# Kernel tuning notes

Hardware: AMD Instinct MI355X
Metric: run time of the kernel (lower is better)

Reference implementation:

```python
import jax, jax.numpy as jnp
import numpy as np

D_MODEL = 512
NUM_HEADS = 8
D_HEAD = D_MODEL // NUM_HEADS
SCALE = 1.0 / np.sqrt(D_HEAD)


def setup_inputs() -> dict:
    key = jax.random.key(0)
    ks = jax.random.split(key, 16)
    B, T, D = 8, 1024, D_MODEL
    std = 1.0 / np.sqrt(D)
    inp = {
        'x': jax.random.normal(ks[0], (B, T, D), jnp.float32),
        'pos_enc': jax.random.normal(ks[1], (1, 2 * T - 1, D), jnp.float32),
        'Wq': jax.random.normal(ks[2], (D, D), jnp.float32) * std,
        'bq': jnp.zeros((D,), jnp.float32),
        'Wk': jax.random.normal(ks[3], (D, D), jnp.float32) * std,
        'bk': jnp.zeros((D,), jnp.float32),
        'Wv': jax.random.normal(ks[4], (D, D), jnp.float32) * std,
        'bv': jnp.zeros((D,), jnp.float32),
        'Wpos': jax.random.normal(ks[5], (D, D), jnp.float32) * std,
        'pos_bias_u': jax.random.normal(ks[6], (NUM_HEADS, D_HEAD), jnp.float32) * std,
        'pos_bias_v': jax.random.normal(ks[7], (NUM_HEADS, D_HEAD), jnp.float32) * std,
        'Wo': jax.random.normal(ks[8], (D, D), jnp.float32) * std,
        'bo': jnp.zeros((D,), jnp.float32),
    }
    return inp


def _relative_shift(x):
    # x: (batch, heads, time, 2*time-1) -> (batch, heads, time, time)
    b, h, t, _ = x.shape
    x = jnp.pad(x, ((0, 0), (0, 0), (0, 0), (1, 0)))  # (b,h,t,2t)
    x = x.reshape(b, h, 2 * t, t)
    x = x[:, :, 1:, :]
    x = x.reshape(b, h, t, 2 * t - 1)
    return x[:, :, :, :t]


def reference(x, pos_enc, Wq, bq, Wk, bk, Wv, bv, Wpos, pos_bias_u, pos_bias_v, Wo, bo):
    B, T, D = x.shape
    H, Dh = NUM_HEADS, D_HEAD
    q = (x @ Wq + bq).reshape(B, T, H, Dh).transpose(0, 2, 1, 3)  # (B,H,T,Dh)
    k = (x @ Wk + bk).reshape(B, T, H, Dh).transpose(0, 2, 1, 3)
    v = (x @ Wv + bv).reshape(B, T, H, Dh).transpose(0, 2, 1, 3)
    p = (pos_enc @ Wpos).reshape(1, -1, H, Dh).transpose(0, 2, 1, 3)  # (1,H,2T-1,Dh)

    q_u = q + pos_bias_u[None, :, None, :]
    q_v = q + pos_bias_v[None, :, None, :]

    content_score = jnp.einsum('bhtd,bhsd->bhts', q_u, k)         # (B,H,T,T)
    pos_score = jnp.einsum('bhtd,xhpd->bhtp', q_v, p)             # (B,H,T,2T-1)
    pos_score = _relative_shift(pos_score)                         # (B,H,T,T)

    scores = (content_score + pos_score) * SCALE
    attn = jax.nn.softmax(scores, axis=-1)
    out = jnp.einsum('bhts,bhsd->bhtd', attn, v)                   # (B,H,T,Dh)
    out = out.transpose(0, 2, 1, 3).reshape(B, T, D)
    return out @ Wo + bo
```

## Files before the change

kernel.cpp:

```cpp
#include <hip/hip_runtime.h>
#include <hip/hip_bf16.h>

#define T_SEQ 1024
#define D_MODEL 512
#define N_HEADS 8
#define D_HEAD 64
#define KSCALE 0.1803368801111244f

typedef unsigned short ushort_t;
typedef short s16x8 __attribute__((ext_vector_type(8)));
typedef float f32x4 __attribute__((ext_vector_type(4)));

__device__ inline f32x4 mfma16(s16x8 a, s16x8 b, f32x4 c) {
    return __builtin_amdgcn_mfma_f32_16x16x32_bf16(a, b, c, 0, 0, 0);
}

__device__ inline ushort_t f2bf(float f) {
    union { float f; unsigned u; } v; v.f = f;
    unsigned r = v.u + 0x7FFFu + ((v.u >> 16) & 1u);
    return (ushort_t)(r >> 16);
}
__device__ inline float bf2f(short s) {
    union { unsigned u; float f; } t; t.u = ((unsigned)(unsigned short)s) << 16; return t.f;
}
__device__ inline void cvt4(const float4 f, ushort_t* t) {
    t[0] = f2bf(f.x); t[1] = f2bf(f.y); t[2] = f2bf(f.z); t[3] = f2bf(f.w);
}
__device__ inline s16x8 pack8(const ushort_t* t) {
    s16x8 r;
    #pragma unroll
    for (int e = 0; e < 8; ++e) r[e] = (short)t[e];
    return r;
}

__device__ inline int lidx(int row, int chunk) {
    return row * 64 + ((chunk ^ (row & 7)) << 3);
}

__device__ inline void gl_lds16(const ushort_t* g, ushort_t* l) {
    __builtin_amdgcn_global_load_lds(
        (const __attribute__((address_space(1))) unsigned*)g,
        (__attribute__((address_space(3))) unsigned*)l, 16, 0, 0);
}

__global__ __launch_bounds__(256) void prep(
    const float* __restrict__ x, const float* __restrict__ pos,
    const float* __restrict__ W0, const float* __restrict__ W1,
    const float* __restrict__ W2, const float* __restrict__ W3,
    const float* __restrict__ W4,
    ushort_t* __restrict__ xb, ushort_t* __restrict__ posb,
    ushort_t* __restrict__ WT)
{
    __shared__ float T[64][68];
    const int bx = blockIdx.x;
    const int tid = threadIdx.x;
    if (bx < 2560) {
        const size_t N1 = (size_t)8192 * 512;
        size_t e = ((size_t)bx * 256 + tid) * 8;
        ushort_t tmp[8];
        if (e < N1) {
            const float4* s = (const float4*)(x + e);
            cvt4(s[0], tmp); cvt4(s[1], tmp + 4);
            *(s16x8*)(xb + e) = pack8(tmp);
        } else {
            size_t e2 = e - N1;
            int row = (int)(e2 >> 9);
            if (row < 2047) {
                const float4* s = (const float4*)(pos + e2);
                cvt4(s[0], tmp); cvt4(s[1], tmp + 4);
            } else {
                #pragma unroll
                for (int i = 0; i < 8; ++i) tmp[i] = 0;
            }
            *(s16x8*)(posb + e2) = pack8(tmp);
        }
    } else {
        const int bz = bx - 2560;
        const int z = bz >> 6;
        const int rem = bz & 63;
        const int n0 = (rem & 7) * 64, k0 = (rem >> 3) * 64;
        const float* W = (z == 0) ? W0 : (z == 1) ? W1
                       : (z == 2) ? W2 : (z == 3) ? W3 : W4;
        const int rr = tid >> 2, cc = (tid & 3) * 16;

        const float* src = W + (size_t)(k0 + rr) * 512 + n0 + cc;
        *(float4*)&T[rr][cc + 0]  = *(const float4*)(src);
        *(float4*)&T[rr][cc + 4]  = *(const float4*)(src + 4);
        *(float4*)&T[rr][cc + 8]  = *(const float4*)(src + 8);
        *(float4*)&T[rr][cc + 12] = *(const float4*)(src + 12);
        __syncthreads();

        ushort_t tmp[16];
        #pragma unroll
        for (int e = 0; e < 16; ++e) tmp[e] = f2bf(T[cc + e][rr]);
        ushort_t* dst = WT + ((size_t)z * 512 + n0 + rr) * 512 + k0 + cc;
        *(s16x8*)dst       = pack8(tmp);
        *(s16x8*)(dst + 8) = pack8(tmp + 8);
    }
}

__global__ __launch_bounds__(256) void gemm_qkvp(
    const ushort_t* __restrict__ xb, const ushort_t* __restrict__ posb,
    const ushort_t* __restrict__ WT,
    const float* __restrict__ bq, const float* __restrict__ bk,
    const float* __restrict__ bv, const float* __restrict__ pbu,
    ushort_t* __restrict__ Qu, ushort_t* __restrict__ Ko,
    ushort_t* __restrict__ VoT, ushort_t* __restrict__ Po)
{
    const int tid = threadIdx.x;
    const int flat = blockIdx.x;
    const int nf = (flat & 7) * 104 + (flat >> 3);
    const int bxi = nf % 13, byi = nf / 13;

    const bool is_p = (bxi == 12);
    int row0, col0;
    const ushort_t* A;
    const ushort_t* B;
    if (is_p) {
        row0 = (byi >> 2) * 128;
        col0 = (byi & 3) * 128;
        A = posb;
        B = WT + (size_t)3 * 512 * 512;
    } else {
        row0 = byi * 128;
        col0 = bxi * 128;
        A = xb;
        B = WT;
    }
    const int w = tid >> 6, lane = tid & 63;
    const int quad = lane >> 4, lanelo = lane & 15;
    const int wr = w >> 1, wc = w & 1;

    __shared__ ushort_t AsF[128 * 64];
    __shared__ ushort_t BsF[128 * 64];

    f32x4 acc[4][4] = {};

    for (int k0 = 0; k0 < 512; k0 += 64) {
        __syncthreads();
        #pragma unroll
        for (int i = 0; i < 4; ++i) {
            const int L = i * 256 + tid;
            const int r = L >> 3, j = (L & 7) * 8;
            ushort_t* lbase = AsF + (size_t)(i * 256 + (tid & ~63)) * 8;
            gl_lds16(A + (size_t)(row0 + r) * 512 + k0 + j, lbase);
            ushort_t* lbase2 = BsF + (size_t)(i * 256 + (tid & ~63)) * 8;
            gl_lds16(B + (size_t)(col0 + r) * 512 + k0 + j, lbase2);
        }
        __syncthreads();

        #pragma unroll
        for (int ks = 0; ks < 2; ++ks) {
            s16x8 af[4], bf[4];
            #pragma unroll
            for (int i = 0; i < 4; ++i)
                af[i] = *(const s16x8*)(AsF + (size_t)(64 * wr + 16 * i + lanelo) * 64 + ks * 32 + quad * 8);
            #pragma unroll
            for (int j = 0; j < 4; ++j)
                bf[j] = *(const s16x8*)(BsF + (size_t)(64 * wc + 16 * j + lanelo) * 64 + ks * 32 + quad * 8);
            #pragma unroll
            for (int i = 0; i < 4; ++i)
                #pragma unroll
                for (int j = 0; j < 4; ++j)
                    acc[i][j] = mfma16(af[i], bf[j], acc[i][j]);
        }
    }

    if (is_p) {
        #pragma unroll
        for (int j = 0; j < 4; ++j) {
            int c = col0 + 64 * wc + 16 * j + lanelo;
            #pragma unroll
            for (int i = 0; i < 4; ++i)
                #pragma unroll
                for (int r = 0; r < 4; ++r) {
                    int row = row0 + 64 * wr + 16 * i + 4 * quad + r;
                    Po[(size_t)row * 512 + c] = f2bf(acc[i][j][r]);
                }
        }
        return;
    }

    const int set = col0 >> 9;
    const int cbase = (col0 & 511) + 64 * wc;
    if (set == 0) {
        #pragma unroll
        for (int j = 0; j < 4; ++j) {
            int c = cbase + 16 * j + lanelo;
            float vq = bq[c] + pbu[c];
            #pragma unroll
            for (int i = 0; i < 4; ++i)
                #pragma unroll
                for (int r = 0; r < 4; ++r) {
                    int row = row0 + 64 * wr + 16 * i + 4 * quad + r;
                    Qu[(size_t)row * 512 + c] = f2bf((acc[i][j][r] + vq) * KSCALE);
                }
        }
    } else if (set == 1) {
        #pragma unroll
        for (int j = 0; j < 4; ++j) {
            int c = cbase + 16 * j + lanelo;
            float vbk = bk[c];
            #pragma unroll
            for (int i = 0; i < 4; ++i)
                #pragma unroll
                for (int r = 0; r < 4; ++r) {
                    int row = row0 + 64 * wr + 16 * i + 4 * quad + r;
                    Ko[(size_t)row * 512 + c] = f2bf(acc[i][j][r] + vbk);
                }
        }
    } else {
        const int b_idx = row0 >> 10;
        #pragma unroll
        for (int j = 0; j < 4; ++j) {
            int c = cbase + 16 * j + lanelo;
            int hh = c >> 6, d = c & 63;
            float vbb = bv[c];
            #pragma unroll
            for (int i = 0; i < 4; ++i) {
                int t = (row0 & 1023) + 64 * wr + 16 * i + 4 * quad;
                ushort4 vp;
                vp.x = f2bf(acc[i][j][0] + vbb);
                vp.y = f2bf(acc[i][j][1] + vbb);
                vp.z = f2bf(acc[i][j][2] + vbb);
                vp.w = f2bf(acc[i][j][3] + vbb);
                *(ushort4*)(VoT + ((size_t)((b_idx * 8 + hh) * 64 + d)) * 1024 + t) = vp;
            }
        }
    }
}

__global__ __launch_bounds__(256, 2) void attn_mfma(
    const ushort_t* __restrict__ Qu,
    const ushort_t* __restrict__ Kb, const ushort_t* __restrict__ VT,
    const ushort_t* __restrict__ Pb,
    const float* __restrict__ pbu, const float* __restrict__ pbv,
    ushort_t* __restrict__ AOb)
{
    const int tid = threadIdx.x;
    const int flat = blockIdx.x;
    const int nf = (flat & 7) * 64 + (flat >> 3);
    const int t0 = (nf & 7) * 128;
    const int h  = (nf >> 3) & 7;
    const int b  = nf >> 6;

    const int w = tid >> 6, lane = tid & 63;
    const int quad = lane >> 4, lanelo = lane & 15;

    __shared__ ushort_t Kt[2 * 64 * 64];
    __shared__ ushort_t VtT[2 * 64 * 64];
    __shared__ ushort_t Pt[256 * 64];
    __shared__ ushort_t Ps[128 * 64];

    const size_t qr0 = (size_t)(b * T_SEQ + t0 + 32 * w + lanelo) * 512 + h * 64;
    s16x8 qu0[2], qu1[2], qv0[2], qv1[2];
    qu0[0] = *(const s16x8*)(Qu + qr0 + quad * 8);
    qu0[1] = *(const s16x8*)(Qu + qr0 + 32 + quad * 8);
    qu1[0] = *(const s16x8*)(Qu + qr0 + (size_t)16 * 512 + quad * 8);
    qu1[1] = *(const s16x8*)(Qu + qr0 + (size_t)16 * 512 + 32 + quad * 8);
    #pragma unroll
    for (int e = 0; e < 8; ++e) {
        int k0i = h * 64 + quad * 8 + e;
        float d0 = (pbv[k0i] - pbu[k0i]) * KSCALE;
        float d1 = (pbv[k0i + 32] - pbu[k0i + 32]) * KSCALE;
        qv0[0][e] = (short)f2bf(bf2f(qu0[0][e]) + d0);
        qv0[1][e] = (short)f2bf(bf2f(qu0[1][e]) + d1);
        qv1[0][e] = (short)f2bf(bf2f(qu1[0][e]) + d0);
        qv1[1][e] = (short)f2bf(bf2f(qu1[1][e]) + d1);
    }

    f32x4 acc_o[2][4] = {};
    float l_part[2][4] = {{0.f,0.f,0.f,0.f},{0.f,0.f,0.f,0.f}};

    const ushort_t* VTbh = VT + ((size_t)((b * 8 + h) * 64)) * 1024;
    const ushort_t* Kbh  = Kb + (size_t)b * T_SEQ * 512 + (size_t)h * 64;
    const int pr_base = 960 - t0;

    {
        #pragma unroll
        for (int i = 0; i < 2; ++i) {
            const int L = i * 256 + tid;
            const int r = L >> 3;
            const int ch = (L & 7) ^ (r & 7);
            gl_lds16(Kbh + (size_t)r * 512 + ch * 8,
                     Kt + (size_t)(i * 256 + (tid & ~63)) * 8);
            gl_lds16(VTbh + (size_t)r * 1024 + ch * 8,
                     VtT + (size_t)(i * 256 + (tid & ~63)) * 8);
        }
        const int g0p = pr_base - 64;
        #pragma unroll
        for (int i = 0; i < 6; ++i) {
            const int L = i * 256 + tid;
            const int gr = g0p + (L >> 3);
            const int ch = (L & 7) ^ (gr & 7);
            const int sgb = (g0p + ((i * 256 + (tid & ~63)) >> 3)) & 255;
            gl_lds16(Pb + (size_t)gr * 512 + h * 64 + ch * 8,
                     Pt + (size_t)sgb * 64);
        }
    }
    __syncthreads();

    for (int it = 0; it < 16; ++it) {
        const int s0 = it * 64;
        const int cur = it & 1;

        if (it < 15) {
            ushort_t* Kn = Kt + (cur ^ 1) * 4096;
            ushort_t* Vn = VtT + (cur ^ 1) * 4096;
            const int sn = s0 + 64;
            #pragma unroll
            for (int i = 0; i < 2; ++i) {
                const int L = i * 256 + tid;
                const int r = L >> 3;
                const int ch = (L & 7) ^ (r & 7);
                gl_lds16(Kbh + (size_t)(sn + r) * 512 + ch * 8,
                         Kn + (size_t)(i * 256 + (tid & ~63)) * 8);
                gl_lds16(VTbh + (size_t)r * 1024 + sn + ch * 8,
                         Vn + (size_t)(i * 256 + (tid & ~63)) * 8);
            }
            const int g0 = pr_base + s0 + 128;
            #pragma unroll
            for (int i = 0; i < 2; ++i) {
                const int L = i * 256 + tid;
                const int gr = g0 + (L >> 3);
                const int ch = (L & 7) ^ (gr & 7);
                const int sgb = (g0 + ((i * 256 + (tid & ~63)) >> 3)) & 255;
                gl_lds16(Pb + (size_t)gr * 512 + h * 64 + ch * 8,
                         Pt + (size_t)sgb * 64);
            }
        }

        const ushort_t* Kc = Kt + cur * 4096;
        const ushort_t* Vc = VtT + cur * 4096;
        const int pb = (pr_base + s0) & 255;

        f32x4 acc_c[2][4] = {};
        f32x4 acc_g[2][5] = {};
        __builtin_amdgcn_s_setprio(1);
        #pragma unroll
        for (int ks = 0; ks < 2; ++ks) {
            #pragma unroll
            for (int tn = 0; tn < 4; ++tn) {
                s16x8 kf = *(const s16x8*)(Kc + lidx(tn * 16 + lanelo, 4 * ks + quad));
                acc_c[0][tn] = mfma16(qu0[ks], kf, acc_c[0][tn]);
                acc_c[1][tn] = mfma16(qu1[ks], kf, acc_c[1][tn]);
            }
            #pragma unroll
            for (int m = 0; m < 6; ++m) {
                int prow = (pb + 256 + (2 - 2 * w + m) * 16 + lanelo) & 255;
                s16x8 pf = *(const s16x8*)(Pt + lidx(prow, 4 * ks + quad));
                if (m >= 1) acc_g[0][m - 1] = mfma16(qv0[ks], pf, acc_g[0][m - 1]);
                if (m <= 4) acc_g[1][m]     = mfma16(qv1[ks], pf, acc_g[1][m]);
            }
        }
        __builtin_amdgcn_s_setprio(0);

        #pragma unroll
        for (int rt = 0; rt < 2; ++rt) {
            #pragma unroll
            for (int r = 0; r < 4; ++r) {
                const int u = lanelo + 15 - 4 * quad - r;
                const int srcl = (quad << 4) | (u & 15);
                const bool hi = (u >= 16);
                #pragma unroll
                for (int tn = 0; tn < 4; ++tn) {
                    float v0 = __shfl(acc_g[rt][tn][r], srcl);
                    float v1 = __shfl(acc_g[rt][tn + 1][r], srcl);
                    float e = __builtin_amdgcn_exp2f(acc_c[rt][tn][r] + (hi ? v1 : v0));
                    l_part[rt][r] += e;
                    const int pr = 32 * w + 16 * rt + 4 * quad + r;
                    const int ch = 2 * tn + (lanelo >> 3);
                    Ps[pr * 64 + ((ch ^ (pr & 7)) << 3) + (lanelo & 7)] = f2bf(e);
                }
            }
        }
        asm volatile("s_waitcnt lgkmcnt(0)" ::: "memory");

        __builtin_amdgcn_s_setprio(1);
        #pragma unroll
        for (int ks = 0; ks < 2; ++ks) {
            s16x8 af0 = *(const s16x8*)(Ps + lidx(32 * w + lanelo, 4 * ks + quad));
            s16x8 af1 = *(const s16x8*)(Ps + lidx(32 * w + 16 + lanelo, 4 * ks + quad));
            #pragma unroll
            for (int dt = 0; dt < 4; ++dt) {
                s16x8 vb = *(const s16x8*)(Vc + lidx(dt * 16 + lanelo, 4 * ks + quad));
                acc_o[0][dt] = mfma16(af0, vb, acc_o[0][dt]);
                acc_o[1][dt] = mfma16(af1, vb, acc_o[1][dt]);
            }
        }
        __builtin_amdgcn_s_setprio(0);

        __syncthreads();
    }

    float inv[2][4];
    #pragma unroll
    for (int rt = 0; rt < 2; ++rt)
        #pragma unroll
        for (int r = 0; r < 4; ++r) {
            float l = l_part[rt][r];
            l += __shfl_xor(l, 1);
            l += __shfl_xor(l, 2);
            l += __shfl_xor(l, 4);
            l += __shfl_xor(l, 8);
            inv[rt][r] = 1.0f / l;
        }

    #pragma unroll
    for (int rt = 0; rt < 2; ++rt)
        #pragma unroll
        for (int dt = 0; dt < 4; ++dt)
            #pragma unroll
            for (int r = 0; r < 4; ++r) {
                const int pr = 32 * w + 16 * rt + 4 * quad + r;
                const int ch = 2 * dt + (lanelo >> 3);
                Ps[pr * 64 + ((ch ^ (pr & 7)) << 3) + (lanelo & 7)] =
                    f2bf(acc_o[rt][dt][r] * inv[rt][r]);
            }
    __syncthreads();
    {
        const int row = tid >> 1, cb = (tid & 1) * 4;
        ushort_t* dst = AOb + (size_t)(b * T_SEQ + t0 + row) * 512 + h * 64 + cb * 8;
        #pragma unroll
        for (int c = 0; c < 4; ++c)
            *(s16x8*)(dst + c * 8) = *(const s16x8*)(Ps + lidx(row, cb + c));
    }
}

__global__ __launch_bounds__(256) void gemm_out(
    const ushort_t* __restrict__ A, const ushort_t* __restrict__ WTo,
    const float* __restrict__ bias, float* __restrict__ C)
{
    const int tid = threadIdx.x;
    const int flat = blockIdx.x;
    const int nfi = (flat & 7) * 32 + (flat >> 3);
    const int col0 = (nfi & 3) * 128;
    const int row0 = (nfi >> 2) * 128;
    const int w = tid >> 6, lane = tid & 63;
    const int quad = lane >> 4, lanelo = lane & 15;
    const int wr = w >> 1, wc = w & 1;

    __shared__ ushort_t AsF[128 * 64];
    __shared__ ushort_t BsF[128 * 64];

    f32x4 acc[4][4] = {};

    for (int k0 = 0; k0 < 512; k0 += 64) {
        __syncthreads();
        #pragma unroll
        for (int i = 0; i < 4; ++i) {
            const int L = i * 256 + tid;
            const int r = L >> 3, j = (L & 7) * 8;
            ushort_t* lbase = AsF + (size_t)(i * 256 + (tid & ~63)) * 8;
            gl_lds16(A + (size_t)(row0 + r) * 512 + k0 + j, lbase);
            ushort_t* lbase2 = BsF + (size_t)(i * 256 + (tid & ~63)) * 8;
            gl_lds16(WTo + (size_t)(col0 + r) * 512 + k0 + j, lbase2);
        }
        __syncthreads();

        #pragma unroll
        for (int ks = 0; ks < 2; ++ks) {
            s16x8 af[4], bf[4];
            #pragma unroll
            for (int i = 0; i < 4; ++i)
                af[i] = *(const s16x8*)(AsF + (size_t)(64 * wr + 16 * i + lanelo) * 64 + ks * 32 + quad * 8);
            #pragma unroll
            for (int j = 0; j < 4; ++j)
                bf[j] = *(const s16x8*)(BsF + (size_t)(64 * wc + 16 * j + lanelo) * 64 + ks * 32 + quad * 8);
            #pragma unroll
            for (int i = 0; i < 4; ++i)
                #pragma unroll
                for (int j = 0; j < 4; ++j)
                    acc[i][j] = mfma16(af[i], bf[j], acc[i][j]);
        }
    }

    #pragma unroll
    for (int j = 0; j < 4; ++j) {
        int c = col0 + 64 * wc + 16 * j + lanelo;
        float vb = bias[c];
        #pragma unroll
        for (int i = 0; i < 4; ++i)
            #pragma unroll
            for (int r = 0; r < 4; ++r) {
                int row = row0 + 64 * wr + 16 * i + 4 * quad + r;
                C[(size_t)row * 512 + c] = acc[i][j][r] + vb;
            }
    }
}

extern "C" void kernel_launch(void* const* d_in, const int* in_sizes, int n_in,
                              void* d_out, int out_size, void* d_ws, size_t ws_size,
                              hipStream_t stream) {
    const float* x       = (const float*)d_in[0];
    const float* pos_enc = (const float*)d_in[1];
    const float* Wq      = (const float*)d_in[2];
    const float* bq      = (const float*)d_in[3];
    const float* Wk      = (const float*)d_in[4];
    const float* bk      = (const float*)d_in[5];
    const float* Wv      = (const float*)d_in[6];
    const float* bv      = (const float*)d_in[7];
    const float* Wpos    = (const float*)d_in[8];
    const float* pbu     = (const float*)d_in[9];
    const float* pbv     = (const float*)d_in[10];
    const float* Wo      = (const float*)d_in[11];
    const float* bo      = (const float*)d_in[12];
    float* out = (float*)d_out;

    const size_t M  = 8 * T_SEQ;
    const size_t SZ = M * D_MODEL;

    char* ws = (char*)d_ws;
    ushort_t* xb   = (ushort_t*)ws;              ws += SZ * 2;
    ushort_t* posb = (ushort_t*)ws;              ws += (size_t)2048 * 512 * 2;
    ushort_t* Qu_b = (ushort_t*)ws;              ws += SZ * 2;
    ushort_t* K_b  = (ushort_t*)ws;              ws += SZ * 2;
    ushort_t* VT_b = (ushort_t*)ws;              ws += SZ * 2;
    ushort_t* P_b  = (ushort_t*)ws;              ws += (size_t)2048 * 512 * 2;
    ushort_t* WT   = (ushort_t*)ws;              ws += (size_t)5 * 512 * 512 * 2;
    ushort_t* AOb  = (ushort_t*)ws;              ws += SZ * 2;

    dim3 blk(256);

    hipLaunchKernelGGL(prep, dim3(2880), blk, 0, stream,
                       x, pos_enc, Wq, Wk, Wv, Wpos, Wo, xb, posb, WT);

    hipLaunchKernelGGL(gemm_qkvp, dim3(832), blk, 0, stream,
                       xb, posb, WT, bq, bk, bv, pbu,
                       Qu_b, K_b, VT_b, P_b);

    hipLaunchKernelGGL(attn_mfma, dim3(512), blk, 0, stream,
                       Qu_b, K_b, VT_b, P_b, pbu, pbv, AOb);

    hipLaunchKernelGGL(gemm_out, dim3(256), blk, 0, stream,
                       AOb, WT + (size_t)4 * 512 * 512, bo, out);
}
```

Baseline: 191.6 us.

## Software-pipeline attention loop: overlap next-tile score MFMAs with current softmax/PV

Result: slower. 306.8 us (+60.1%).

```diff
diff --git a/kernel.cpp b/kernel.cpp
--- a/kernel.cpp
+++ b/kernel.cpp
@@ -230,6 +230,124 @@
     }
 }
 
+__device__ __attribute__((always_inline)) inline void stage_k(
+    const ushort_t* Kbh, ushort_t* Kd, int sn, int tid)
+{
+    #pragma unroll
+    for (int i = 0; i < 2; ++i) {
+        const int L = i * 256 + tid;
+        const int r = L >> 3;
+        const int ch = (L & 7) ^ (r & 7);
+        gl_lds16(Kbh + (size_t)(sn + r) * 512 + ch * 8,
+                 Kd + (size_t)(i * 256 + (tid & ~63)) * 8);
+    }
+}
+__device__ __attribute__((always_inline)) inline void stage_v(
+    const ushort_t* VTbh, ushort_t* Vd, int sn, int tid)
+{
+    #pragma unroll
+    for (int i = 0; i < 2; ++i) {
+        const int L = i * 256 + tid;
+        const int r = L >> 3;
+        const int ch = (L & 7) ^ (r & 7);
+        gl_lds16(VTbh + (size_t)r * 1024 + sn + ch * 8,
+                 Vd + (size_t)(i * 256 + (tid & ~63)) * 8);
+    }
+}
+__device__ __attribute__((always_inline)) inline void stage_p(
+    const ushort_t* Pb, ushort_t* Pt, int g0, int hoff, int tid)
+{
+    #pragma unroll
+    for (int i = 0; i < 2; ++i) {
+        const int L = i * 256 + tid;
+        const int gr = g0 + (L >> 3);
+        const int ch = (L & 7) ^ (gr & 7);
+        const int sgb = (g0 + ((i * 256 + (tid & ~63)) >> 3)) & 255;
+        gl_lds16(Pb + (size_t)gr * 512 + hoff + ch * 8,
+                 Pt + (size_t)sgb * 64);
+    }
+}
+
+__device__ __attribute__((always_inline)) inline void score_blk(
+    f32x4 (&cc)[2][4], f32x4 (&gg)[2][5],
+    const ushort_t* Kc, const ushort_t* Pt, int pbn,
+    const s16x8 (&qu0)[2], const s16x8 (&qu1)[2],
+    const s16x8 (&qv0)[2], const s16x8 (&qv1)[2],
+    int w, int quad, int lanelo)
+{
+    #pragma unroll
+    for (int rt = 0; rt < 2; ++rt) {
+        #pragma unroll
+        for (int tn = 0; tn < 4; ++tn) cc[rt][tn] = (f32x4){0.f, 0.f, 0.f, 0.f};
+        #pragma unroll
+        for (int m = 0; m < 5; ++m) gg[rt][m] = (f32x4){0.f, 0.f, 0.f, 0.f};
+    }
+    __builtin_amdgcn_s_setprio(1);
+    #pragma unroll
+    for (int ks = 0; ks < 2; ++ks) {
+        #pragma unroll
+        for (int tn = 0; tn < 4; ++tn) {
+            s16x8 kf = *(const s16x8*)(Kc + lidx(tn * 16 + lanelo, 4 * ks + quad));
+            cc[0][tn] = mfma16(qu0[ks], kf, cc[0][tn]);
+            cc[1][tn] = mfma16(qu1[ks], kf, cc[1][tn]);
+        }
+        #pragma unroll
+        for (int m = 0; m < 6; ++m) {
+            int prow = (pbn + 256 + (2 - 2 * w + m) * 16 + lanelo) & 255;
+            s16x8 pf = *(const s16x8*)(Pt + lidx(prow, 4 * ks + quad));
+            if (m >= 1) gg[0][m - 1] = mfma16(qv0[ks], pf, gg[0][m - 1]);
+            if (m <= 4) gg[1][m]     = mfma16(qv1[ks], pf, gg[1][m]);
+        }
+    }
+    __builtin_amdgcn_s_setprio(0);
+}
+
+__device__ __attribute__((always_inline)) inline void extract_blk(
+    const f32x4 (&cc)[2][4], const f32x4 (&gg)[2][5],
+    ushort_t* Ps, float (&l_part)[2][4],
+    int w, int quad, int lanelo)
+{
+    #pragma unroll
+    for (int rt = 0; rt < 2; ++rt) {
+        #pragma unroll
+        for (int r = 0; r < 4; ++r) {
+            const int u = lanelo + 15 - 4 * quad - r;
+            const int srcl = (quad << 4) | (u & 15);
+            const bool hi = (u >= 16);
+            #pragma unroll
+            for (int tn = 0; tn < 4; ++tn) {
+                float v0 = __shfl(gg[rt][tn][r], srcl);
+                float v1 = __shfl(gg[rt][tn + 1][r], srcl);
+                float e = __builtin_amdgcn_exp2f(cc[rt][tn][r] + (hi ? v1 : v0));
+                l_part[rt][r] += e;
+                const int pr = 32 * w + 16 * rt + 4 * quad + r;
+                const int ch = 2 * tn + (lanelo >> 3);
+                Ps[pr * 64 + ((ch ^ (pr & 7)) << 3) + (lanelo & 7)] = f2bf(e);
+            }
+        }
+    }
+}
+
+__device__ __attribute__((always_inline)) inline void pv_blk(
+    f32x4 (&acc_o)[2][4], const ushort_t* Ps, const ushort_t* Vc,
+    int w, int quad, int lanelo)
+{
+    asm volatile("s_waitcnt lgkmcnt(0)" ::: "memory");
+    __builtin_amdgcn_s_setprio(1);
+    #pragma unroll
+    for (int ks = 0; ks < 2; ++ks) {
+        s16x8 af0 = *(const s16x8*)(Ps + lidx(32 * w + lanelo, 4 * ks + quad));
+        s16x8 af1 = *(const s16x8*)(Ps + lidx(32 * w + 16 + lanelo, 4 * ks + quad));
+        #pragma unroll
+        for (int dt = 0; dt < 4; ++dt) {
+            s16x8 vb = *(const s16x8*)(Vc + lidx(dt * 16 + lanelo, 4 * ks + quad));
+            acc_o[0][dt] = mfma16(af0, vb, acc_o[0][dt]);
+            acc_o[1][dt] = mfma16(af1, vb, acc_o[1][dt]);
+        }
+    }
+    __builtin_amdgcn_s_setprio(0);
+}
+
 __global__ __launch_bounds__(256, 2) void attn_mfma(
     const ushort_t* __restrict__ Qu,
     const ushort_t* __restrict__ Kb, const ushort_t* __restrict__ VT,
@@ -275,123 +393,52 @@
     const ushort_t* VTbh = VT + ((size_t)((b * 8 + h) * 64)) * 1024;
     const ushort_t* Kbh  = Kb + (size_t)b * T_SEQ * 512 + (size_t)h * 64;
     const int pr_base = 960 - t0;
-
-    {
-        #pragma unroll
-        for (int i = 0; i < 2; ++i) {
-            const int L = i * 256 + tid;
-            const int r = L >> 3;
-            const int ch = (L & 7) ^ (r & 7);
-            gl_lds16(Kbh + (size_t)r * 512 + ch * 8,
-                     Kt + (size_t)(i * 256 + (tid & ~63)) * 8);
-            gl_lds16(VTbh + (size_t)r * 1024 + ch * 8,
-                     VtT + (size_t)(i * 256 + (tid & ~63)) * 8);
-        }
-        const int g0p = pr_base - 64;
-        #pragma unroll
-        for (int i = 0; i < 6; ++i) {
-            const int L = i * 256 + tid;
-            const int gr = g0p + (L >> 3);
-            const int ch = (L & 7) ^ (gr & 7);
-            const int sgb = (g0p + ((i * 256 + (tid & ~63)) >> 3)) & 255;
-            gl_lds16(Pb + (size_t)gr * 512 + h * 64 + ch * 8,
-                     Pt + (size_t)sgb * 64);
-        }
-    }
+    const int hoff = h * 64;
+
+    stage_k(Kbh, Kt, 0, tid);
+    stage_k(Kbh, Kt + 4096, 64, tid);
+    stage_v(VTbh, VtT, 0, tid);
+    stage_p(Pb, Pt, pr_base - 64, hoff, tid);
+    stage_p(Pb, Pt, pr_base,       hoff, tid);
+    stage_p(Pb, Pt, pr_base + 64,  hoff, tid);
+    stage_p(Pb, Pt, pr_base + 128, hoff, tid);
     __syncthreads();
 
-    for (int it = 0; it < 16; ++it) {
-        const int s0 = it * 64;
-        const int cur = it & 1;
-
-        if (it < 15) {
-            ushort_t* Kn = Kt + (cur ^ 1) * 4096;
-            ushort_t* Vn = VtT + (cur ^ 1) * 4096;
-            const int sn = s0 + 64;
-            #pragma unroll
-            for (int i = 0; i < 2; ++i) {
-                const int L = i * 256 + tid;
-                const int r = L >> 3;
-                const int ch = (L & 7) ^ (r & 7);
-                gl_lds16(Kbh + (size_t)(sn + r) * 512 + ch * 8,
-                         Kn + (size_t)(i * 256 + (tid & ~63)) * 8);
-                gl_lds16(VTbh + (size_t)r * 1024 + sn + ch * 8,
-                         Vn + (size_t)(i * 256 + (tid & ~63)) * 8);
-            }
-            const int g0 = pr_base + s0 + 128;
-            #pragma unroll
-            for (int i = 0; i < 2; ++i) {
-                const int L = i * 256 + tid;
-                const int gr = g0 + (L >> 3);
-                const int ch = (L & 7) ^ (gr & 7);
-                const int sgb = (g0 + ((i * 256 + (tid & ~63)) >> 3)) & 255;
-                gl_lds16(Pb + (size_t)gr * 512 + h * 64 + ch * 8,
-                         Pt + (size_t)sgb * 64);
-            }
-        }
-
-        const ushort_t* Kc = Kt + cur * 4096;
-        const ushort_t* Vc = VtT + cur * 4096;
-        const int pb = (pr_base + s0) & 255;
-
-        f32x4 acc_c[2][4] = {};
-        f32x4 acc_g[2][5] = {};
-        __builtin_amdgcn_s_setprio(1);
-        #pragma unroll
-        for (int ks = 0; ks < 2; ++ks) {
-            #pragma unroll
-            for (int tn = 0; tn < 4; ++tn) {
-                s16x8 kf = *(const s16x8*)(Kc + lidx(tn * 16 + lanelo, 4 * ks + quad));
-                acc_c[0][tn] = mfma16(qu0[ks], kf, acc_c[0][tn]);
-                acc_c[1][tn] = mfma16(qu1[ks], kf, acc_c[1][tn]);
-            }
-            #pragma unroll
-            for (int m = 0; m < 6; ++m) {
-                int prow = (pb + 256 + (2 - 2 * w + m) * 16 + lanelo) & 255;
-                s16x8 pf = *(const s16x8*)(Pt + lidx(prow, 4 * ks + quad));
-                if (m >= 1) acc_g[0][m - 1] = mfma16(qv0[ks], pf, acc_g[0][m - 1]);
-                if (m <= 4) acc_g[1][m]     = mfma16(qv1[ks], pf, acc_g[1][m]);
-            }
-        }
-        __builtin_amdgcn_s_setprio(0);
-
-        #pragma unroll
-        for (int rt = 0; rt < 2; ++rt) {
-            #pragma unroll
-            for (int r = 0; r < 4; ++r) {
-                const int u = lanelo + 15 - 4 * quad - r;
-                const int srcl = (quad << 4) | (u & 15);
-                const bool hi = (u >= 16);
-                #pragma unroll
-                for (int tn = 0; tn < 4; ++tn) {
-                    float v0 = __shfl(acc_g[rt][tn][r], srcl);
-                    float v1 = __shfl(acc_g[rt][tn + 1][r], srcl);
-                    float e = __builtin_amdgcn_exp2f(acc_c[rt][tn][r] + (hi ? v1 : v0));
-                    l_part[rt][r] += e;
-                    const int pr = 32 * w + 16 * rt + 4 * quad + r;
-                    const int ch = 2 * tn + (lanelo >> 3);
-                    Ps[pr * 64 + ((ch ^ (pr & 7)) << 3) + (lanelo & 7)] = f2bf(e);
-                }
-            }
-        }
-        asm volatile("s_waitcnt lgkmcnt(0)" ::: "memory");
-
-        __builtin_amdgcn_s_setprio(1);
-        #pragma unroll
-        for (int ks = 0; ks < 2; ++ks) {
-            s16x8 af0 = *(const s16x8*)(Ps + lidx(32 * w + lanelo, 4 * ks + quad));
-            s16x8 af1 = *(const s16x8*)(Ps + lidx(32 * w + 16 + lanelo, 4 * ks + quad));
-            #pragma unroll
-            for (int dt = 0; dt < 4; ++dt) {
-                s16x8 vb = *(const s16x8*)(Vc + lidx(dt * 16 + lanelo, 4 * ks + quad));
-                acc_o[0][dt] = mfma16(af0, vb, acc_o[0][dt]);
-                acc_o[1][dt] = mfma16(af1, vb, acc_o[1][dt]);
-            }
-        }
-        __builtin_amdgcn_s_setprio(0);
-
-        __syncthreads();
-    }
+    f32x4 c0[2][4], g0a[2][5], c1[2][4], g1a[2][5];
+    score_blk(c0, g0a, Kt, Pt, pr_base & 255, qu0, qu1, qv0, qv1, w, quad, lanelo);
+
+    for (int it2 = 0; it2 < 7; ++it2) {
+        {
+            const int sA = it2 * 128;
+            stage_k(Kbh, Kt, sA + 128, tid);
+            stage_v(VTbh, VtT + 4096, sA + 64, tid);
+            stage_p(Pb, Pt, pr_base + sA + 192, hoff, tid);
+            score_blk(c1, g1a, Kt + 4096, Pt, (pr_base + sA + 64) & 255,
+                      qu0, qu1, qv0, qv1, w, quad, lanelo);
+            extract_blk(c0, g0a, Ps, l_part, w, quad, lanelo);
+            pv_blk(acc_o, Ps, VtT, w, quad, lanelo);
+            __syncthreads();
+        }
+        {
+            const int sB = it2 * 128 + 64;
+            stage_k(Kbh, Kt + 4096, sB + 128, tid);
+            stage_v(VTbh, VtT, sB + 64, tid);
+            stage_p(Pb, Pt, pr_base + sB + 192, hoff, tid);
+            score_blk(c0, g0a, Kt, Pt, (pr_base + sB + 64) & 255,
+                      qu0, qu1, qv0, qv1, w, quad, lanelo);
+            extract_blk(c1, g1a, Ps, l_part, w, quad, lanelo);
+            pv_blk(acc_o, Ps, VtT + 4096, w, quad, lanelo);
+            __syncthreads();
+        }
+    }
+    stage_v(VTbh, VtT + 4096, 960, tid);
+    score_blk(c1, g1a, Kt + 4096, Pt, (pr_base + 960) & 255,
+              qu0, qu1, qv0, qv1, w, quad, lanelo);
+    extract_blk(c0, g0a, Ps, l_part, w, quad, lanelo);
+    pv_blk(acc_o, Ps, VtT, w, quad, lanelo);
+    __syncthreads();
+    extract_blk(c1, g1a, Ps, l_part, w, quad, lanelo);
+    pv_blk(acc_o, Ps, VtT + 4096, w, quad, lanelo);
 
     float inv[2][4];
     #pragma unroll
@@ -406,6 +453,7 @@
             inv[rt][r] = 1.0f / l;
         }
 
+    __syncthreads();
     #pragma unroll
     for (int rt = 0; rt < 2; ++rt)
         #pragma unroll
```
